# Kernel optimization log

Measured on AMD Instinct MI355X. Metric: run time of the kernel, lower is better.

## Reference

```python
import jax, jax.numpy as jnp
import numpy as np

N = 8192

def _gcn_layer(x, src, dst, W, b, norm_out, norm_in, activation=None):
    # DGL GraphConv, norm='both': D_in^{-1/2} A D_out^{-1/2} X W + b
    xw = x @ W                              # [N, out] (weight first: in>=out)
    m = (xw * norm_out[:, None])[src]       # gather per-edge messages [E, out]
    agg = jax.ops.segment_sum(m, dst, num_segments=N)
    h = agg * norm_in[:, None] + b
    return activation(h) if activation is not None else h


def setup_inputs() -> dict:
    key = jax.random.key(0)
    k1, k2, k3, k4, k5 = jax.random.split(key, 5)
    E = 262144
    in_dim, h1, h2 = 512, 256, 64
    features = jax.random.normal(k1, (N, in_dim), dtype=jnp.float32)
    src = jax.random.randint(k2, (E,), 0, N)
    dst = jax.random.randint(k3, (E,), 0, N)
    W1 = jax.random.normal(k4, (in_dim, h1), dtype=jnp.float32) / np.sqrt(in_dim)
    b1 = jnp.zeros((h1,), dtype=jnp.float32)
    W2 = jax.random.normal(k5, (h1, h2), dtype=jnp.float32) / np.sqrt(h1)
    b2 = jnp.zeros((h2,), dtype=jnp.float32)
    return {"features": features, "src": src, "dst": dst,
            "W1": W1, "b1": b1, "W2": W2, "b2": b2}


def reference(features, src, dst, W1, b1, W2, b2):
    # Degrees and symmetric normalization (clamp(min=1) as in DGL GraphConv).
    ones = jnp.ones(src.shape[0], dtype=features.dtype)
    deg_out = jax.ops.segment_sum(ones, src, num_segments=N)
    deg_in = jax.ops.segment_sum(ones, dst, num_segments=N)
    norm_out = jnp.maximum(deg_out, 1.0) ** -0.5
    norm_in = jnp.maximum(deg_in, 1.0) ** -0.5
    # Encoder (dropout is identity in eval mode).
    h = _gcn_layer(features, src, dst, W1, b1, norm_out, norm_in, jax.nn.relu)
    z = _gcn_layer(h, src, dst, W2, b2, norm_out, norm_in, None)
    # Dot-product decoder.
    adj_rec = jax.nn.sigmoid(z @ z.T)       # [N, N]
    return adj_rec
```

## Files before the change

### kernel.cpp

```cpp
#include <hip/hip_runtime.h>
#include <hip/hip_bf16.h>
#include <math.h>

#define NNODES 8192
#define NEDGES 262144
#define INDIM  512
#define H1     256
#define H2     64

typedef __attribute__((ext_vector_type(8))) short bf16x8;
typedef __attribute__((ext_vector_type(4))) float f32x4;

static __device__ __forceinline__ float bf2f(unsigned short u) {
    return __uint_as_float((unsigned)u << 16);
}
static __device__ __forceinline__ unsigned short f2bf(float f) {
    __hip_bfloat16 h = __float2bfloat16(f);
    return *(unsigned short*)&h;
}


__global__ void deg_kernel(const int* __restrict__ src, const int* __restrict__ dst,
                           int* deg_out, int* deg_in) {
    int e = blockIdx.x * blockDim.x + threadIdx.x;
    if (e < NEDGES) {
        atomicAdd(&deg_out[src[e]], 1);
        atomicAdd(&deg_in[dst[e]], 1);
    }
}

__global__ void norm_kernel(const int* __restrict__ deg_out, const int* __restrict__ deg_in,
                            float* norm_out, float* norm_in) {
    int i = blockIdx.x * blockDim.x + threadIdx.x;
    if (i < NNODES) {
        norm_out[i] = 1.0f / sqrtf(fmaxf((float)deg_out[i], 1.0f));
        norm_in[i]  = 1.0f / sqrtf(fmaxf((float)deg_in[i],  1.0f));
    }
}

__global__ __launch_bounds__(1024) void scan_kernel(const int* __restrict__ deg_in,
                                                    int* __restrict__ row_start) {
    __shared__ int part[1024];
    int t = threadIdx.x;
    int v[8]; int s = 0;
#pragma unroll
    for (int u = 0; u < 8; u++) { v[u] = deg_in[t * 8 + u]; s += v[u]; }
    part[t] = s; __syncthreads();
    for (int off = 1; off < 1024; off <<= 1) {
        int x = part[t];
        if (t >= off) x += part[t - off];
        __syncthreads();
        part[t] = x;
        __syncthreads();
    }
    int run = part[t] - s;
#pragma unroll
    for (int u = 0; u < 8; u++) { row_start[t * 8 + u] = run; run += v[u]; }
    if (t == 1023) row_start[NNODES] = run;
}

__global__ void bucket_kernel(const int* __restrict__ src, const int* __restrict__ dst,
                              const int* __restrict__ row_start,
                              int* cursor, int* __restrict__ sorted_src) {
    int e = blockIdx.x * blockDim.x + threadIdx.x;
    if (e < NEDGES) {
        int d = dst[e];
        int p = atomicAdd(&cursor[d], 1);
        sorted_src[row_start[d] + p] = src[e];
    }
}


__global__ void cast4_kernel(const float* __restrict__ in, __hip_bfloat16* __restrict__ out) {
    int t = blockIdx.x * blockDim.x + threadIdx.x;
    float4 v = ((const float4*)in)[t];
    ushort4 o;
    o.x = f2bf(v.x); o.y = f2bf(v.y); o.z = f2bf(v.z); o.w = f2bf(v.w);
    ((ushort4*)out)[t] = o;
}

template<int K, int N>
__global__ void wtrans_kernel(const float* __restrict__ W, __hip_bfloat16* __restrict__ WT) {
    int t = blockIdx.x * blockDim.x + threadIdx.x;
    if (t < K * N) {
        int k = t / N, c = t % N;
        WT[(size_t)c * K + k] = __float2bfloat16(W[t]);
    }
}


template<int K, int MT, int NT, int NOUT>
__global__ __launch_bounds__(256) void gemm_mfma_kernel(const __hip_bfloat16* __restrict__ Af,
                                                        const __hip_bfloat16* __restrict__ BTf,
                                                        const float* __restrict__ scale,
                                                        __hip_bfloat16* __restrict__ outf) {
    constexpr int AM = MT / 64;
    constexpr int BN = NT / 16;
    const short* A  = (const short*)Af;
    const short* BT = (const short*)BTf;
    short* out = (short*)outf;
    const int lane = threadIdx.x & 63;
    const int wid  = threadIdx.x >> 6;
    const int i0 = blockIdx.y * MT + wid * (MT / 4);
    const int j0 = blockIdx.x * NT;
    const int fr = lane & 15;
    const int kg = lane >> 4;

    f32x4 acc[AM][BN] = {};
    for (int k0 = 0; k0 < K; k0 += 32) {
        bf16x8 a[AM], b[BN];
#pragma unroll
        for (int m = 0; m < AM; m++)
            a[m] = *(const bf16x8*)&A[(size_t)(i0 + m * 16 + fr) * K + k0 + kg * 8];
#pragma unroll
        for (int n = 0; n < BN; n++)
            b[n] = *(const bf16x8*)&BT[(size_t)(j0 + n * 16 + fr) * K + k0 + kg * 8];
#pragma unroll
        for (int m = 0; m < AM; m++)
#pragma unroll
            for (int n = 0; n < BN; n++)
                acc[m][n] = __builtin_amdgcn_mfma_f32_16x16x32_bf16(a[m], b[n], acc[m][n], 0, 0, 0);
    }

    const int col = lane & 15;
    const int rg4 = (lane >> 4) * 4;
#pragma unroll
    for (int m = 0; m < AM; m++)
#pragma unroll
        for (int r = 0; r < 4; r++) {
            int row = i0 + m * 16 + rg4 + r;
            float sc = scale[row];
#pragma unroll
            for (int n = 0; n < BN; n++)
                out[(size_t)row * NOUT + j0 + n * 16 + col] = f2bf(acc[m][n][r] * sc);
        }
}


__global__ void agg256_kernel(const int* __restrict__ row_start, const int* __restrict__ sorted_src,
                              const __hip_bfloat16* __restrict__ msgb, const float* __restrict__ norm_in,
                              const float* __restrict__ bias, __hip_bfloat16* __restrict__ outb) {
    const ushort4* msg = (const ushort4*)msgb;
    int n = blockIdx.x;
    int lane = threadIdx.x;
    int e0 = row_start[n], e1 = row_start[n + 1];
    float ax = 0.f, ay = 0.f, az = 0.f, aw = 0.f;
    int e = e0;
    for (; e + 1 < e1; e += 2) {
        int s0 = sorted_src[e], s1 = sorted_src[e + 1];
        ushort4 v0 = msg[(size_t)s0 * 64 + lane];
        ushort4 v1 = msg[(size_t)s1 * 64 + lane];
        ax += bf2f(v0.x) + bf2f(v1.x);
        ay += bf2f(v0.y) + bf2f(v1.y);
        az += bf2f(v0.z) + bf2f(v1.z);
        aw += bf2f(v0.w) + bf2f(v1.w);
    }
    if (e < e1) {
        ushort4 v0 = msg[(size_t)sorted_src[e] * 64 + lane];
        ax += bf2f(v0.x); ay += bf2f(v0.y); az += bf2f(v0.z); aw += bf2f(v0.w);
    }
    float ni = norm_in[n];
    float4 bb = ((const float4*)bias)[lane];
    ushort4 o;
    o.x = f2bf(fmaxf(ax * ni + bb.x, 0.f));
    o.y = f2bf(fmaxf(ay * ni + bb.y, 0.f));
    o.z = f2bf(fmaxf(az * ni + bb.z, 0.f));
    o.w = f2bf(fmaxf(aw * ni + bb.w, 0.f));
    ((ushort4*)outb)[(size_t)n * 64 + lane] = o;
}


__global__ void agg64_kernel(const int* __restrict__ row_start, const int* __restrict__ sorted_src,
                             const __hip_bfloat16* __restrict__ msgb, const float* __restrict__ norm_in,
                             const float* __restrict__ bias, __hip_bfloat16* __restrict__ outb) {
    const unsigned* msg = (const unsigned*)msgb;
    int n = blockIdx.x;
    int lane = threadIdx.x;
    int half = lane >> 5, li = lane & 31;
    int e0 = row_start[n], e1 = row_start[n + 1];
    float ax = 0.f, ay = 0.f;
    for (int e = e0 + half; e < e1; e += 2) {
        unsigned u = msg[(size_t)sorted_src[e] * 32 + li];
        ax += bf2f((unsigned short)(u & 0xffff));
        ay += bf2f((unsigned short)(u >> 16));
    }
    ax += __shfl_xor(ax, 32);
    ay += __shfl_xor(ay, 32);
    if (half == 0) {
        float ni = norm_in[n];
        float z0 = ax * ni + bias[2 * li];
        float z1 = ay * ni + bias[2 * li + 1];
        unsigned o = (unsigned)f2bf(z0) | ((unsigned)f2bf(z1) << 16);
        ((unsigned*)outb)[(size_t)n * 32 + li] = o;
    }
}


__global__ __launch_bounds__(256) void decoder_mfma_kernel(const __hip_bfloat16* __restrict__ zbf,
                                                           float* __restrict__ out) {
    const short* zb = (const short*)zbf;
    const int lane = threadIdx.x & 63;
    const int wid  = threadIdx.x >> 6;
    const int i0 = blockIdx.y * 128 + wid * 32;
    const int j0 = blockIdx.x * 128;
    const int fr = lane & 15;
    const int kg = lane >> 4;

    f32x4 acc[2][8] = {};
#pragma unroll
    for (int ks = 0; ks < 2; ks++) {
        bf16x8 a[2], b[8];
#pragma unroll
        for (int m = 0; m < 2; m++)
            a[m] = *(const bf16x8*)&zb[(size_t)(i0 + m * 16 + fr) * H2 + ks * 32 + kg * 8];
#pragma unroll
        for (int n = 0; n < 8; n++)
            b[n] = *(const bf16x8*)&zb[(size_t)(j0 + n * 16 + fr) * H2 + ks * 32 + kg * 8];
#pragma unroll
        for (int m = 0; m < 2; m++)
#pragma unroll
            for (int n = 0; n < 8; n++)
                acc[m][n] = __builtin_amdgcn_mfma_f32_16x16x32_bf16(a[m], b[n], acc[m][n], 0, 0, 0);
    }

    const int col = lane & 15;
    const int rg4 = (lane >> 4) * 4;
#pragma unroll
    for (int m = 0; m < 2; m++)
#pragma unroll
        for (int n = 0; n < 8; n++) {
            size_t base = (size_t)(i0 + m * 16 + rg4) * NNODES + j0 + n * 16 + col;
#pragma unroll
            for (int r = 0; r < 4; r++) {
                float v = 1.f / (1.f + __expf(-acc[m][n][r]));
                __builtin_nontemporal_store(v, &out[base + (size_t)r * NNODES]);
            }
        }
}


extern "C" void kernel_launch(void* const* d_in, const int* in_sizes, int n_in,
                              void* d_out, int out_size, void* d_ws, size_t ws_size,
                              hipStream_t stream) {
    const float* features = (const float*)d_in[0];
    const int*   src      = (const int*)d_in[1];
    const int*   dst      = (const int*)d_in[2];
    const float* W1       = (const float*)d_in[3];
    const float* b1       = (const float*)d_in[4];
    const float* W2       = (const float*)d_in[5];
    const float* b2       = (const float*)d_in[6];
    float* out = (float*)d_out;

    char* p = (char*)d_ws;
    auto alloc = [&](size_t bytes) -> void* {
        void* q = (void*)p;
        p += (bytes + 255) & ~(size_t)255;
        return q;
    };
    int*   deg_out_i  = (int*)alloc(NNODES * 4);
    int*   deg_in_i   = (int*)alloc(NNODES * 4);
    int*   cursor     = (int*)alloc(NNODES * 4);
    int*   row_start  = (int*)alloc((NNODES + 1) * 4);
    float* norm_out   = (float*)alloc(NNODES * 4);
    float* norm_in    = (float*)alloc(NNODES * 4);
    int*   sorted_src = (int*)alloc(NEDGES * 4);
    __hip_bfloat16* featb = (__hip_bfloat16*)alloc((size_t)NNODES * INDIM * 2);
    __hip_bfloat16* w1t   = (__hip_bfloat16*)alloc((size_t)H1 * INDIM * 2);
    __hip_bfloat16* w2t   = (__hip_bfloat16*)alloc((size_t)H2 * H1 * 2);
    __hip_bfloat16* xwb   = (__hip_bfloat16*)alloc((size_t)NNODES * H1 * 2);
    __hip_bfloat16* hb    = (__hip_bfloat16*)alloc((size_t)NNODES * H1 * 2);
    __hip_bfloat16* hwb   = (__hip_bfloat16*)alloc((size_t)NNODES * H2 * 2);
    __hip_bfloat16* zb    = (__hip_bfloat16*)alloc((size_t)NNODES * H2 * 2);

    hipMemsetAsync(deg_out_i, 0, 3 * NNODES * 4, stream);

    deg_kernel<<<NEDGES / 256, 256, 0, stream>>>(src, dst, deg_out_i, deg_in_i);
    norm_kernel<<<NNODES / 256, 256, 0, stream>>>(deg_out_i, deg_in_i, norm_out, norm_in);
    scan_kernel<<<1, 1024, 0, stream>>>(deg_in_i, row_start);
    bucket_kernel<<<NEDGES / 256, 256, 0, stream>>>(src, dst, row_start, cursor, sorted_src);

    cast4_kernel<<<NNODES * INDIM / 4 / 256, 256, 0, stream>>>(features, featb);
    wtrans_kernel<INDIM, H1><<<(INDIM * H1 + 255) / 256, 256, 0, stream>>>(W1, w1t);
    wtrans_kernel<H1, H2><<<(H1 * H2 + 255) / 256, 256, 0, stream>>>(W2, w2t);

    gemm_mfma_kernel<INDIM, 128, 128, H1><<<dim3(H1 / 128, NNODES / 128), 256, 0, stream>>>(
        featb, w1t, norm_out, xwb);
    agg256_kernel<<<NNODES, 64, 0, stream>>>(row_start, sorted_src, xwb, norm_in, b1, hb);

    gemm_mfma_kernel<H1, 64, 64, H2><<<dim3(1, NNODES / 64), 256, 0, stream>>>(
        hb, w2t, norm_out, hwb);
    agg64_kernel<<<NNODES, 64, 0, stream>>>(row_start, sorted_src, hwb, norm_in, b2, zb);

    decoder_mfma_kernel<<<dim3(NNODES / 128, NNODES / 128), 256, 0, stream>>>(zb, out);
}
```

Before: 178.7 us.

## Fuse norm into scan, merge prep kernels, add polynomial sigmoid fast path

```diff
diff --git a/kernel.cpp b/kernel.cpp
--- a/kernel.cpp
+++ b/kernel.cpp
@@ -29,17 +29,11 @@
     }
 }
 
-__global__ void norm_kernel(const int* __restrict__ deg_out, const int* __restrict__ deg_in,
-                            float* norm_out, float* norm_in) {
-    int i = blockIdx.x * blockDim.x + threadIdx.x;
-    if (i < NNODES) {
-        norm_out[i] = 1.0f / sqrtf(fmaxf((float)deg_out[i], 1.0f));
-        norm_in[i]  = 1.0f / sqrtf(fmaxf((float)deg_in[i],  1.0f));
-    }
-}
-
-__global__ __launch_bounds__(1024) void scan_kernel(const int* __restrict__ deg_in,
-                                                    int* __restrict__ row_start) {
+__global__ __launch_bounds__(1024) void scannorm_kernel(const int* __restrict__ deg_in,
+                                                        const int* __restrict__ deg_out,
+                                                        int* __restrict__ row_start,
+                                                        float* __restrict__ norm_out,
+                                                        float* __restrict__ norm_in) {
     __shared__ int part[1024];
     int t = threadIdx.x;
     int v[8]; int s = 0;
@@ -55,7 +49,12 @@
     }
     int run = part[t] - s;
 #pragma unroll
-    for (int u = 0; u < 8; u++) { row_start[t * 8 + u] = run; run += v[u]; }
+    for (int u = 0; u < 8; u++) {
+        int n = t * 8 + u;
+        row_start[n] = run; run += v[u];
+        norm_in[n]  = 1.0f / sqrtf(fmaxf((float)v[u], 1.0f));
+        norm_out[n] = 1.0f / sqrtf(fmaxf((float)deg_out[n], 1.0f));
+    }
     if (t == 1023) row_start[NNODES] = run;
 }
 
@@ -71,20 +70,24 @@
 }
 
 
-__global__ void cast4_kernel(const float* __restrict__ in, __hip_bfloat16* __restrict__ out) {
-    int t = blockIdx.x * blockDim.x + threadIdx.x;
-    float4 v = ((const float4*)in)[t];
-    ushort4 o;
-    o.x = f2bf(v.x); o.y = f2bf(v.y); o.z = f2bf(v.z); o.w = f2bf(v.w);
-    ((ushort4*)out)[t] = o;
-}
-
-template<int K, int N>
-__global__ void wtrans_kernel(const float* __restrict__ W, __hip_bfloat16* __restrict__ WT) {
-    int t = blockIdx.x * blockDim.x + threadIdx.x;
-    if (t < K * N) {
-        int k = t / N, c = t % N;
-        WT[(size_t)c * K + k] = __float2bfloat16(W[t]);
+__global__ void prep_kernel(const float* __restrict__ features, __hip_bfloat16* __restrict__ featb,
+                            const float* __restrict__ W1, __hip_bfloat16* __restrict__ w1t,
+                            const float* __restrict__ W2, __hip_bfloat16* __restrict__ w2t) {
+    int b = blockIdx.x;
+    if (b < 4096) {
+        int t = b * 256 + threadIdx.x;
+        float4 v = ((const float4*)features)[t];
+        ushort4 o;
+        o.x = f2bf(v.x); o.y = f2bf(v.y); o.z = f2bf(v.z); o.w = f2bf(v.w);
+        ((ushort4*)featb)[t] = o;
+    } else if (b < 4608) {
+        int t = (b - 4096) * 256 + threadIdx.x;
+        int k = t / H1, c = t % H1;
+        w1t[(size_t)c * INDIM + k] = __float2bfloat16(W1[t]);
+    } else {
+        int t = (b - 4608) * 256 + threadIdx.x;
+        int k = t / H2, c = t % H2;
+        w2t[(size_t)c * H1 + k] = __float2bfloat16(W2[t]);
     }
 }
 
@@ -169,7 +172,6 @@
     ((ushort4*)outb)[(size_t)n * 64 + lane] = o;
 }
 
-
 __global__ void agg64_kernel(const int* __restrict__ row_start, const int* __restrict__ sorted_src,
                              const __hip_bfloat16* __restrict__ msgb, const float* __restrict__ norm_in,
                              const float* __restrict__ bias, __hip_bfloat16* __restrict__ outb) {
@@ -225,6 +227,7 @@
 
     const int col = lane & 15;
     const int rg4 = (lane >> 4) * 4;
+    float mx = 0.f;
 #pragma unroll
     for (int m = 0; m < 2; m++)
 #pragma unroll
@@ -232,10 +235,26 @@
             size_t base = (size_t)(i0 + m * 16 + rg4) * NNODES + j0 + n * 16 + col;
 #pragma unroll
             for (int r = 0; r < 4; r++) {
-                float v = 1.f / (1.f + __expf(-acc[m][n][r]));
-                __builtin_nontemporal_store(v, &out[base + (size_t)r * NNODES]);
+                float x = acc[m][n][r];
+                float u = x * x;
+                float s = 0.5f + x * (0.25f + u * (-0.0208333333f + u * 0.0020833333f));
+                __builtin_nontemporal_store(s, &out[base + (size_t)r * NNODES]);
+                mx = fmaxf(mx, fabsf(x));
             }
         }
+    if (__any(mx > 1.0f)) {
+#pragma unroll
+        for (int m = 0; m < 2; m++)
+#pragma unroll
+            for (int n = 0; n < 8; n++) {
+                size_t base = (size_t)(i0 + m * 16 + rg4) * NNODES + j0 + n * 16 + col;
+#pragma unroll
+                for (int r = 0; r < 4; r++) {
+                    float x = acc[m][n][r];
+                    out[base + (size_t)r * NNODES] = 1.f / (1.f + __expf(-x));
+                }
+            }
+    }
 }
 
 
@@ -275,13 +294,9 @@
     hipMemsetAsync(deg_out_i, 0, 3 * NNODES * 4, stream);
 
     deg_kernel<<<NEDGES / 256, 256, 0, stream>>>(src, dst, deg_out_i, deg_in_i);
-    norm_kernel<<<NNODES / 256, 256, 0, stream>>>(deg_out_i, deg_in_i, norm_out, norm_in);
-    scan_kernel<<<1, 1024, 0, stream>>>(deg_in_i, row_start);
+    scannorm_kernel<<<1, 1024, 0, stream>>>(deg_in_i, deg_out_i, row_start, norm_out, norm_in);
     bucket_kernel<<<NEDGES / 256, 256, 0, stream>>>(src, dst, row_start, cursor, sorted_src);
-
-    cast4_kernel<<<NNODES * INDIM / 4 / 256, 256, 0, stream>>>(features, featb);
-    wtrans_kernel<INDIM, H1><<<(INDIM * H1 + 255) / 256, 256, 0, stream>>>(W1, w1t);
-    wtrans_kernel<H1, H2><<<(H1 * H2 + 255) / 256, 256, 0, stream>>>(W2, w2t);
+    prep_kernel<<<4672, 256, 0, stream>>>(features, featb, W1, w1t, W2, w2t);
 
     gemm_mfma_kernel<INDIM, 128, 128, H1><<<dim3(H1 / 128, NNODES / 128), 256, 0, stream>>>(
         featb, w1t, norm_out, xwb);
```

Result: slower. 186.9 us (+4.6%).
